# Kernel tuning notes

Measured on AMD Instinct MI355X. Metric: run time of the kernel, lower is better.

The kernel has to match this reference:

```python
import jax, jax.numpy as jnp
import numpy as np
from jax import lax

SEGMENTS = 64
KERNEL = 5


def setup_inputs() -> dict:
    key = jax.random.key(0)
    k1, k2, k3 = jax.random.split(key, 3)
    B, S, F = 4, 4096, 1024
    A6 = 512 * 6
    inp = jax.random.normal(k1, (B, S, F), dtype=jnp.float32)
    W = jax.random.normal(k2, (A6, F), dtype=jnp.float32) * (1.0 / np.sqrt(F))
    b = jax.random.normal(k3, (A6,), dtype=jnp.float32) * 0.01
    return {"inp": inp, "W": W, "b": b}


def reference(inp, W, b):
    # Fused projection: [B,S,F] @ [F,6A] -> [B,S,6A]
    x = jnp.einsum('bsf,af->bsa', inp, W) + b
    qry, key, val, seg, loc, out = jnp.split(x, 6, axis=2)  # each [B,S,A]
    B, S, A = out.shape

    # Global aggregated attention branch
    agg = qry.mean(axis=1)                              # [B,A]
    scores = jnp.einsum('ba,bsa->bs', agg, key)         # [B,S]
    w = jax.nn.softmax(scores, axis=1)                  # [B,S]
    ctx = jnp.einsum('bs,bsa->ba', w, val)              # [B,A]
    aggregated = ctx[:, None, :] * out                  # [B,S,A]

    # Segment max-pool branch
    nseg = S // SEGMENTS
    seg4 = seg.reshape(B, nseg, SEGMENTS, A)
    seg_max = seg4.max(axis=2, keepdims=True)           # [B,nseg,1,A]
    segment_max_pooled = (seg_max * out.reshape(B, nseg, SEGMENTS, A)).reshape(B, S, A)

    # Local sliding-window max-pool branch (stride 1, pad KERNEL//2, -inf padding)
    pad = KERNEL // 2
    local_max_pooled = lax.reduce_window(
        loc, -jnp.inf, lax.max,
        window_dimensions=(1, KERNEL, 1),
        window_strides=(1, 1, 1),
        padding=((0, 0), (pad, pad), (0, 0)))           # [B,S,A]

    return aggregated + segment_max_pooled + local_max_pooled
```

## Files before the change

### kernel.cpp

```cpp
#include <hip/hip_runtime.h>
#include <hip/hip_bf16.h>
#include <stdint.h>

#define B_    4
#define S_    4096
#define F_    1024
#define A_    512
#define N3_   1536
#define M_    16384

#define BM    256
#define BK    64
#define NT    (F_ / BK)
#define LDP   266

typedef __attribute__((ext_vector_type(8))) __bf16 bf16x8;
typedef __attribute__((ext_vector_type(4))) float  f32x4;

#define MFMA(a, b, c) __builtin_amdgcn_mfma_f32_16x16x32_bf16((a), (b), (c), 0, 0, 0)

__device__ __forceinline__ float bflo(unsigned int u) {
  union { unsigned int i; float f; } v; v.i = u << 16; return v.f;
}
__device__ __forceinline__ float bfhi(unsigned int u) {
  union { unsigned int i; float f; } v; v.i = u & 0xffff0000u; return v.f;
}
__device__ __forceinline__ float bf1(unsigned short u) {
  union { unsigned int i; float f; } v; v.i = ((unsigned int)u) << 16; return v.f;
}
__device__ __forceinline__ unsigned short bfc(float f) {
  return __builtin_bit_cast(unsigned short, __float2bfloat16(f));
}

__device__ __forceinline__ ushort4 cvt_bf4(float4 v) {
  ushort4 o;
  o.x = bfc(v.x); o.y = bfc(v.y); o.z = bfc(v.z); o.w = bfc(v.w);
  return o;
}

typedef __attribute__((address_space(3))) unsigned int lds_uint;
typedef const __attribute__((address_space(1))) unsigned int glob_uint;
__device__ __forceinline__ void lds_load16(const void* g, void* l) {
  __builtin_amdgcn_global_load_lds((glob_uint*)g, (lds_uint*)l, 16, 0, 0);
}

__global__ __launch_bounds__(256) void convert_mean_kernel(
    const float* __restrict__ inp, const float* __restrict__ W,
    unsigned short* __restrict__ inp_bf, unsigned short* __restrict__ w_bf,
    float* __restrict__ mu) {
  int blk = blockIdx.x;
  int t   = threadIdx.x;
  int r0  = blk * 32;
  int b   = r0 >> 12;
  float acc0 = 0.f, acc1 = 0.f, acc2 = 0.f, acc3 = 0.f;
  for (int r = 0; r < 32; r++) {
    size_t row = (size_t)(r0 + r);
    float4 v = ((const float4*)(inp + row * F_))[t];
    acc0 += v.x; acc1 += v.y; acc2 += v.z; acc3 += v.w;
    ((ushort4*)(inp_bf + row * F_))[t] = cvt_bf4(v);
  }
  atomicAdd(&mu[b * F_ + t * 4 + 0], acc0);
  atomicAdd(&mu[b * F_ + t * 4 + 1], acc1);
  atomicAdd(&mu[b * F_ + t * 4 + 2], acc2);
  atomicAdd(&mu[b * F_ + t * 4 + 3], acc3);

  const float* Wc = W + (size_t)N3_ * F_;
  const int n4 = (N3_ * F_) / 4;
  for (int i = blk * 256 + t; i < n4; i += 512 * 256) {
    ((ushort4*)w_bf)[i] = cvt_bf4(((const float4*)Wc)[i]);
  }
}

__global__ void agg_kernel(const float* __restrict__ mu, const float* __restrict__ W,
                           const float* __restrict__ bias, float* __restrict__ agg) {
  int gw = blockIdx.x * 4 + (threadIdx.x >> 6);
  int lane = threadIdx.x & 63;
  int b = gw >> 9, a = gw & 511;
  const float4* wr = (const float4*)(W + (size_t)a * F_);
  const float4* mr = (const float4*)(mu + b * F_);
  float s = 0.f;
#pragma unroll
  for (int k = 0; k < 4; k++) {
    float4 wv = wr[lane + 64 * k], mv = mr[lane + 64 * k];
    s += wv.x * mv.x + wv.y * mv.y + wv.z * mv.z + wv.w * mv.w;
  }
  for (int off = 32; off; off >>= 1) s += __shfl_down(s, off);
  if (lane == 0) agg[b * A_ + a] = s * (1.f / S_) + bias[a];
}

__global__ void v_kernel(const float* __restrict__ agg, const float* __restrict__ W,
                         const float* __restrict__ bias, float* __restrict__ v,
                         float* __restrict__ cvec) {
  int fc = blockIdx.x;
  int ac = blockIdx.y;
  int t = threadIdx.x;
  int f = fc * 256 + t;
  const float* Wk = W + (size_t)A_ * F_;
  float s0 = 0.f, s1 = 0.f, s2 = 0.f, s3 = 0.f;
  int a0 = ac * 64;
  for (int a = a0; a < a0 + 64; a++) {
    float wv = Wk[(size_t)a * F_ + f];
    s0 += agg[a] * wv;
    s1 += agg[A_ + a] * wv;
    s2 += agg[2 * A_ + a] * wv;
    s3 += agg[3 * A_ + a] * wv;
  }
  atomicAdd(&v[f], s0);
  atomicAdd(&v[F_ + f], s1);
  atomicAdd(&v[2 * F_ + f], s2);
  atomicAdd(&v[3 * F_ + f], s3);

  if (fc == 0 && ac == 0) {
    int bb = t >> 6, l = t & 63;
    float c = 0.f;
#pragma unroll
    for (int i = 0; i < 8; i++) c += agg[bb * A_ + l + 64 * i] * bias[A_ + l + 64 * i];
    for (int off = 32; off; off >>= 1) c += __shfl_down(c, off);
    if (l == 0) cvec[bb] = c;
  }
}

__global__ void scores_kernel(const unsigned short* __restrict__ inp_bf,
                              const float* __restrict__ v,
                              const float* __restrict__ cvec, float* __restrict__ scores) {
  int lane = threadIdx.x & 63;
  int row = blockIdx.x * 4 + (threadIdx.x >> 6);
  int b = row >> 12;
  const uint4* ip = (const uint4*)(inp_bf + (size_t)row * F_);
  const float4* vp = (const float4*)(v + b * F_);
  float s = 0.f;
#pragma unroll
  for (int k = 0; k < 2; k++) {
    uint4 x = ip[lane + 64 * k];
    float4 va = vp[(lane + 64 * k) * 2];
    float4 vb = vp[(lane + 64 * k) * 2 + 1];
    s += bflo(x.x) * va.x + bfhi(x.x) * va.y + bflo(x.y) * va.z + bfhi(x.y) * va.w +
         bflo(x.z) * vb.x + bfhi(x.z) * vb.y + bflo(x.w) * vb.z + bfhi(x.w) * vb.w;
  }
  for (int off = 32; off; off >>= 1) s += __shfl_down(s, off);
  if (lane == 0) scores[row] = s + cvec[b];
}

__global__ void softmax_kernel(float* __restrict__ sc) {
  __shared__ float red[256];
  int b = blockIdx.x, t = threadIdx.x;
  float* p = sc + b * S_;
  float vals[16];
  float m = -1e30f;
#pragma unroll
  for (int i = 0; i < 16; i++) { vals[i] = p[t + i * 256]; m = fmaxf(m, vals[i]); }
  red[t] = m; __syncthreads();
  for (int o = 128; o; o >>= 1) { if (t < o) red[t] = fmaxf(red[t], red[t + o]); __syncthreads(); }
  m = red[0]; __syncthreads();
  float sum = 0.f;
#pragma unroll
  for (int i = 0; i < 16; i++) { vals[i] = __expf(vals[i] - m); sum += vals[i]; }
  red[t] = sum; __syncthreads();
  for (int o = 128; o; o >>= 1) { if (t < o) red[t] += red[t + o]; __syncthreads(); }
  float inv = 1.f / red[0];
#pragma unroll
  for (int i = 0; i < 16; i++) p[t + i * 256] = vals[i] * inv;
}

__global__ void u_kernel(const unsigned short* __restrict__ inp_bf,
                         const float* __restrict__ w, float* __restrict__ u) {
  int b = blockIdx.z, fc = blockIdx.y, sc = blockIdx.x;
  int t = threadIdx.x;
  int f2 = fc * 512 + t * 2;
  int s0 = sc * 128;
  const float* wp = w + b * S_ + s0;
  const unsigned short* ip = inp_bf + ((size_t)(b * S_ + s0)) * F_ + f2;
  float a0 = 0.f, a1 = 0.f;
  for (int s = 0; s < 128; s++) {
    unsigned int xv = *(const unsigned int*)&ip[(size_t)s * F_];
    float ws = wp[s];
    a0 += ws * bflo(xv);
    a1 += ws * bfhi(xv);
  }
  atomicAdd(&u[b * F_ + f2], a0);
  atomicAdd(&u[b * F_ + f2 + 1], a1);
}

__global__ void ctx_kernel(const float* __restrict__ u, const float* __restrict__ W,
                           const float* __restrict__ bias, float* __restrict__ ctx) {
  int gw = blockIdx.x * 4 + (threadIdx.x >> 6);
  int lane = threadIdx.x & 63;
  int b = gw >> 9, a = gw & 511;
  const float4* wr = (const float4*)(W + (size_t)(2 * A_ + a) * F_);
  const float4* ur = (const float4*)(u + b * F_);
  float s = 0.f;
#pragma unroll
  for (int k = 0; k < 4; k++) {
    float4 wv = wr[lane + 64 * k], uv = ur[lane + 64 * k];
    s += wv.x * uv.x + wv.y * uv.y + wv.z * uv.z + wv.w * uv.w;
  }
  for (int off = 32; off; off >>= 1) s += __shfl_down(s, off);
  if (lane == 0) ctx[b * A_ + a] = s + bias[2 * A_ + a];
}

__global__ __launch_bounds__(512, 2) void gemm_fused(
    const __hip_bfloat16* __restrict__ Abf,
    const __hip_bfloat16* __restrict__ Wbf,
    const float* __restrict__ biasP,
    const float* __restrict__ ctx,
    float* __restrict__ out,
    unsigned short* __restrict__ sideLoc,
    float* __restrict__ sideGO) {
  extern __shared__ unsigned short smem[];
  unsigned short* ldsA = smem;
  unsigned short* ldsB = smem + 32768;
  unsigned short* Xt   = smem;
  float* segred = (float*)((char*)smem + 192 * LDP * 2);

  int bid = blockIdx.x;
  int swz = (bid & 7) * 64 + (bid >> 3);
  int mb = swz >> 3;
  int nb = swz & 7;

  int tid  = threadIdx.x;
  int lane = tid & 63;
  int wv   = tid >> 6;
  int wm   = wv >> 1;
  int wn   = wv & 1;
  int lo   = lane & 15, hi = lane >> 4, sw = lane & 7;

  int bir0 = (((hi * 16)      ^ (sw << 4)) >> 1);
  int bir1 = (((64 + hi * 16) ^ (sw << 4)) >> 1);

  const __hip_bfloat16* Ab = Abf + (size_t)mb * BM * F_;

  int srow = tid >> 3;
  int sel  = ((tid & 7) ^ (srow & 7)) * 8;
  int ldst = wv * 512;

  f32x4 acc[4][6];
#pragma unroll
  for (int i = 0; i < 4; i++)
#pragma unroll
    for (int j = 0; j < 6; j++) acc[i][j] = (f32x4){0.f, 0.f, 0.f, 0.f};

  int aBase = (wm * 64 + lo) * 64;
  int bBase = (wn * 96 + lo) * 64;

#define STG_A(kt_, buf_, r_)                                                              \
  lds_load16(Ab + (size_t)((r_) * 64 + srow) * F_ + (kt_) * BK + sel,                     \
             ldsA + (buf_) * 16384 + (r_) * 4096 + ldst)
#define STG_B(kt_, buf_, q_)                                                              \
  lds_load16(Wbf + (size_t)((q_) * 512 + nb * 64 + srow) * F_ + (kt_) * BK + sel,         \
             ldsB + (buf_) * 12288 + (q_) * 4096 + ldst)

  bf16x8 af[4][2], b01[2][2], b23[2][2], b45[2][2];

  STG_A(0, 0, 0); STG_A(0, 0, 1); STG_A(0, 0, 2); STG_A(0, 0, 3);
  STG_B(0, 0, 0); STG_B(0, 0, 1); STG_B(0, 0, 2);
  asm volatile("s_waitcnt vmcnt(0)" ::: "memory");
  __builtin_amdgcn_s_barrier();
#pragma unroll
  for (int i = 0; i < 4; i++) {
    af[i][0] = *(const bf16x8*)&ldsA[aBase + i * 1024 + bir0];
    af[i][1] = *(const bf16x8*)&ldsA[aBase + i * 1024 + bir1];
  }
#pragma unroll
  for (int j = 0; j < 2; j++) {
    b01[j][0] = *(const bf16x8*)&ldsB[bBase + j * 1024 + bir0];
    b01[j][1] = *(const bf16x8*)&ldsB[bBase + j * 1024 + bir1];
  }

  for (int kt = 0; kt < NT; ++kt) {
    int c = kt & 1, nx = c ^ 1;
    bool pf = (kt + 1 < NT);
    const unsigned short* lb  = ldsB + c * 12288;
    const unsigned short* lan = ldsA + nx * 16384;
    const unsigned short* lbn = ldsB + nx * 12288;

    if (pf) { STG_A(kt + 1, nx, 0); STG_A(kt + 1, nx, 1); STG_A(kt + 1, nx, 2); STG_A(kt + 1, nx, 3); }
    asm volatile("s_waitcnt lgkmcnt(0)" ::: "memory");
    __builtin_amdgcn_sched_barrier(0);
    __builtin_amdgcn_s_setprio(1);
#pragma unroll
    for (int i = 0; i < 4; i++)
#pragma unroll
      for (int j = 0; j < 2; j++) {
        acc[i][j] = MFMA(af[i][0], b01[j][0], acc[i][j]);
        acc[i][j] = MFMA(af[i][1], b01[j][1], acc[i][j]);
      }
    __builtin_amdgcn_s_setprio(0);
#pragma unroll
    for (int j = 0; j < 2; j++) {
      b23[j][0] = *(const bf16x8*)&lb[bBase + (2 + j) * 1024 + bir0];
      b23[j][1] = *(const bf16x8*)&lb[bBase + (2 + j) * 1024 + bir1];
    }
    __builtin_amdgcn_s_barrier();

    if (pf) { STG_B(kt + 1, nx, 0); STG_B(kt + 1, nx, 1); STG_B(kt + 1, nx, 2); }
    asm volatile("s_waitcnt lgkmcnt(0)" ::: "memory");
    __builtin_amdgcn_sched_barrier(0);
    __builtin_amdgcn_s_setprio(1);
#pragma unroll
    for (int i = 0; i < 4; i++)
#pragma unroll
      for (int j = 0; j < 2; j++) {
        acc[i][2 + j] = MFMA(af[i][0], b23[j][0], acc[i][2 + j]);
        acc[i][2 + j] = MFMA(af[i][1], b23[j][1], acc[i][2 + j]);
      }
    __builtin_amdgcn_s_setprio(0);
#pragma unroll
    for (int j = 0; j < 2; j++) {
      b45[j][0] = *(const bf16x8*)&lb[bBase + (4 + j) * 1024 + bir0];
      b45[j][1] = *(const bf16x8*)&lb[bBase + (4 + j) * 1024 + bir1];
    }
    __builtin_amdgcn_s_barrier();

    asm volatile("s_waitcnt lgkmcnt(0)" ::: "memory");
    __builtin_amdgcn_sched_barrier(0);
    __builtin_amdgcn_s_setprio(1);
#pragma unroll
    for (int i = 0; i < 4; i++)
#pragma unroll
      for (int j = 0; j < 2; j++) {
        acc[i][4 + j] = MFMA(af[i][0], b45[j][0], acc[i][4 + j]);
        acc[i][4 + j] = MFMA(af[i][1], b45[j][1], acc[i][4 + j]);
      }
    __builtin_amdgcn_s_setprio(0);
    if (pf) asm volatile("s_waitcnt vmcnt(0)" ::: "memory");
    __builtin_amdgcn_s_barrier();
    if (pf) {
#pragma unroll
      for (int i = 0; i < 4; i++) {
        af[i][0] = *(const bf16x8*)&lan[aBase + i * 1024 + bir0];
        af[i][1] = *(const bf16x8*)&lan[aBase + i * 1024 + bir1];
      }
#pragma unroll
      for (int j = 0; j < 2; j++) {
        b01[j][0] = *(const bf16x8*)&lbn[bBase + j * 1024 + bir0];
        b01[j][1] = *(const bf16x8*)&lbn[bBase + j * 1024 + bir1];
      }
    }
  }
#undef STG_A
#undef STG_B

  float bias_r[6];
#pragma unroll
  for (int fj = 0; fj < 6; fj++) {
    int cl = wn * 96 + fj * 16 + lo;
    bias_r[fj] = biasP[(cl >> 6) * 512 + nb * 64 + (cl & 63)];
  }
#pragma unroll
  for (int fi = 0; fi < 4; fi++) {
#pragma unroll
    for (int fj = 0; fj < 6; fj++) {
      int cl = wn * 96 + fj * 16 + lo;
      int r  = wm * 64 + fi * 16 + hi * 4;
      float v0 = acc[fi][fj][0] + bias_r[fj];
      float v1 = acc[fi][fj][1] + bias_r[fj];
      float v2 = acc[fi][fj][2] + bias_r[fj];
      float v3 = acc[fi][fj][3] + bias_r[fj];
      unsigned int u01 = (unsigned int)bfc(v0) | ((unsigned int)bfc(v1) << 16);
      unsigned int u23 = (unsigned int)bfc(v2) | ((unsigned int)bfc(v3) << 16);
      *(unsigned int*)&Xt[cl * LDP + r]     = u01;
      *(unsigned int*)&Xt[cl * LDP + r + 2] = u23;
    }
  }
  __syncthreads();

  if (tid < 256) {
    int seg = tid >> 6, c = tid & 63;
    int base = c * LDP + seg * 64;
    float m = -1e30f;
#pragma unroll
    for (int k = 0; k < 32; k++) {
      unsigned int u = *(const unsigned int*)&Xt[base + 2 * k];
      m = fmaxf(m, fmaxf(bflo(u), bfhi(u)));
    }
    segred[seg * 64 + c] = m;
  }
  __syncthreads();

  {
    int c  = lane;
    int r0 = wv * 32;
    int b  = mb >> 4;
    int gcol = nb * 64 + c;
    float g = ctx[b * 512 + gcol] + segred[(r0 >> 6) * 64 + c];
    int lbase = (64 + c) * LDP;
    int obase = (128 + c) * LDP;
    float lw0 = bf1(Xt[lbase + max(r0 - 2, 0)]);
    float lw1 = bf1(Xt[lbase + max(r0 - 1, 0)]);
    float lw2 = bf1(Xt[lbase + r0]);
    float lw3 = bf1(Xt[lbase + r0 + 1]);
    size_t obase_g = ((size_t)(mb * 256 + r0)) * 512 + gcol;
#pragma unroll
    for (int j = 0; j < 32; j++) {
      int rn = min(r0 + j + 2, 255);
      float lw4 = bf1(Xt[lbase + rn]);
      float lm = fmaxf(fmaxf(fmaxf(lw0, lw1), fmaxf(lw2, lw3)), lw4);
      float o = bf1(Xt[obase + r0 + j]);
      out[obase_g + (size_t)j * 512] = g * o + lm;
      lw0 = lw1; lw1 = lw2; lw2 = lw3; lw3 = lw4;
    }
  }

  if (tid < 256) {
    int rsel = tid >> 6, c = tid & 63;
    int r = (rsel < 2) ? rsel : (252 + rsel);
    int b = mb >> 4;
    float g = ctx[b * 512 + nb * 64 + c] + segred[(r >> 6) * 64 + c];
    float o = bf1(Xt[(128 + c) * LDP + r]);
    int gr = mb * 4 + rsel;
    sideLoc[gr * 512 + nb * 64 + c] = Xt[(64 + c) * LDP + r];
    sideGO[gr * 512 + nb * 64 + c]  = g * o;
  }
}

__global__ void fixup_kernel(const unsigned short* __restrict__ sideLoc,
                             const float* __restrict__ sideGO,
                             float* __restrict__ out) {
  int rb = blockIdx.x;
  int tb = rb & 15;
  int t = threadIdx.x;
  int rsel = t >> 6, cq = t & 63;
#pragma unroll
  for (int k = 0; k < 8; k++) {
    int c = cq * 8 + k;
    float miss;
    int rl;
    if (rsel == 0) {
      if (tb == 0) continue;
      miss = fmaxf(bf1(sideLoc[((rb - 1) * 4 + 2) * 512 + c]),
                   bf1(sideLoc[((rb - 1) * 4 + 3) * 512 + c]));
      rl = 0;
    } else if (rsel == 1) {
      if (tb == 0) continue;
      miss = bf1(sideLoc[((rb - 1) * 4 + 3) * 512 + c]);
      rl = 1;
    } else if (rsel == 2) {
      if (tb == 15) continue;
      miss = bf1(sideLoc[((rb + 1) * 4 + 0) * 512 + c]);
      rl = 254;
    } else {
      if (tb == 15) continue;
      miss = fmaxf(bf1(sideLoc[((rb + 1) * 4 + 0) * 512 + c]),
                   bf1(sideLoc[((rb + 1) * 4 + 1) * 512 + c]));
      rl = 255;
    }
    size_t oi = ((size_t)rb * 256 + rl) * 512 + c;
    float cand = sideGO[(rb * 4 + rsel) * 512 + c] + miss;
    out[oi] = fmaxf(out[oi], cand);
  }
}

extern "C" void kernel_launch(void* const* d_in, const int* in_sizes, int n_in,
                              void* d_out, int out_size, void* d_ws, size_t ws_size,
                              hipStream_t stream) {
  const float* inp  = (const float*)d_in[0];
  const float* W    = (const float*)d_in[1];
  const float* bias = (const float*)d_in[2];
  float* out = (float*)d_out;
  char* ws = (char*)d_ws;

  const size_t INP_OFF  = 0;
  const size_t W_OFF    = 33554432;
  const size_t MU_OFF   = 36700160;
  const size_t U_OFF    = MU_OFF + 16384;
  const size_t V_OFF    = U_OFF + 16384;
  const size_t CV_OFF   = V_OFF + 16384;
  const size_t AGG_OFF  = CV_OFF + 256;
  const size_t CTX_OFF  = AGG_OFF + 8192;
  const size_t SC_OFF   = CTX_OFF + 8192;
  const size_t SL_OFF   = SC_OFF + 65536;
  const size_t SG_OFF   = SL_OFF + 262144;

  unsigned short* inp_bf = (unsigned short*)(ws + INP_OFF);
  unsigned short* w_bf   = (unsigned short*)(ws + W_OFF);
  float* mu     = (float*)(ws + MU_OFF);
  float* u      = (float*)(ws + U_OFF);
  float* v      = (float*)(ws + V_OFF);
  float* cvec   = (float*)(ws + CV_OFF);
  float* agg    = (float*)(ws + AGG_OFF);
  float* ctx    = (float*)(ws + CTX_OFF);
  float* scores = (float*)(ws + SC_OFF);
  unsigned short* sideLoc = (unsigned short*)(ws + SL_OFF);
  float* sideGO = (float*)(ws + SG_OFF);

  hipFuncSetAttribute(reinterpret_cast<const void*>(gemm_fused),
                      hipFuncAttributeMaxDynamicSharedMemorySize, 114688);

  hipMemsetAsync(ws + MU_OFF, 0, 3 * 16384 + 256, stream);
  convert_mean_kernel<<<512, 256, 0, stream>>>(inp, W, inp_bf, w_bf, mu);
  agg_kernel<<<512, 256, 0, stream>>>(mu, W, bias, agg);
  v_kernel<<<dim3(4, 8), 256, 0, stream>>>(agg, W, bias, v, cvec);
  scores_kernel<<<4096, 256, 0, stream>>>(inp_bf, v, cvec, scores);
  softmax_kernel<<<4, 256, 0, stream>>>(scores);
  u_kernel<<<dim3(32, 2, 4), 256, 0, stream>>>(inp_bf, scores, u);
  ctx_kernel<<<512, 256, 0, stream>>>(u, W, bias, ctx);
  gemm_fused<<<512, 512, 114688, stream>>>((const __hip_bfloat16*)inp_bf,
                                           (const __hip_bfloat16*)w_bf,
                                           bias + 3 * A_, ctx, out, sideLoc, sideGO);
  fixup_kernel<<<64, 256, 0, stream>>>(sideLoc, sideGO, out);
}
```

Baseline: 126.8 us.

## Fuse scores, softmax and weighted sum into chunked online-softmax kernels

Replaces the separate scores, softmax and u kernels with a per-chunk kernel that computes scores, a local max/exp and a partial weighted sum. A small combine kernel then rescales the partials with a global max and normaliser. The per-batch bias constant is dropped because softmax ignores a constant shift. This removes one full pass over the bf16 input, the 4-block serial softmax and the atomics. The cost is an extra partial buffer and a combine step.

```diff
diff --git a/kernel.cpp b/kernel.cpp
--- a/kernel.cpp
+++ b/kernel.cpp
@@ -15,9 +15,9 @@
 #define LDP   266
 
 typedef __attribute__((ext_vector_type(8))) __bf16 bf16x8;
-typedef __attribute__((ext_vector_type(4))) float  f32x4;
 
 #define MFMA(a, b, c) __builtin_amdgcn_mfma_f32_16x16x32_bf16((a), (b), (c), 0, 0, 0)
+typedef __attribute__((ext_vector_type(4))) float f32x4;
 
 __device__ __forceinline__ float bflo(unsigned int u) {
   union { unsigned int i; float f; } v; v.i = u << 16; return v.f;
@@ -31,7 +31,6 @@
 __device__ __forceinline__ unsigned short bfc(float f) {
   return __builtin_bit_cast(unsigned short, __float2bfloat16(f));
 }
-
 __device__ __forceinline__ ushort4 cvt_bf4(float4 v) {
   ushort4 o;
   o.x = bfc(v.x); o.y = bfc(v.y); o.z = bfc(v.z); o.w = bfc(v.w);
@@ -89,8 +88,7 @@
 }
 
 __global__ void v_kernel(const float* __restrict__ agg, const float* __restrict__ W,
-                         const float* __restrict__ bias, float* __restrict__ v,
-                         float* __restrict__ cvec) {
+                         float* __restrict__ v) {
   int fc = blockIdx.x;
   int ac = blockIdx.y;
   int t = threadIdx.x;
@@ -109,76 +107,77 @@
   atomicAdd(&v[F_ + f], s1);
   atomicAdd(&v[2 * F_ + f], s2);
   atomicAdd(&v[3 * F_ + f], s3);
-
-  if (fc == 0 && ac == 0) {
-    int bb = t >> 6, l = t & 63;
-    float c = 0.f;
-#pragma unroll
-    for (int i = 0; i < 8; i++) c += agg[bb * A_ + l + 64 * i] * bias[A_ + l + 64 * i];
-    for (int off = 32; off; off >>= 1) c += __shfl_down(c, off);
-    if (l == 0) cvec[bb] = c;
-  }
-}
-
-__global__ void scores_kernel(const unsigned short* __restrict__ inp_bf,
-                              const float* __restrict__ v,
-                              const float* __restrict__ cvec, float* __restrict__ scores) {
-  int lane = threadIdx.x & 63;
-  int row = blockIdx.x * 4 + (threadIdx.x >> 6);
-  int b = row >> 12;
-  const uint4* ip = (const uint4*)(inp_bf + (size_t)row * F_);
+}
+
+__global__ __launch_bounds__(256) void scores_u_kernel(
+    const unsigned short* __restrict__ inp_bf, const float* __restrict__ v,
+    float* __restrict__ uP, float* __restrict__ mlzl) {
+  int blk = blockIdx.x;
+  int b = blk >> 6, ch = blk & 63;
+  int s0 = ch * 64;
+  int t = threadIdx.x, lane = t & 63, wv = t >> 6;
+  __shared__ float sc[64];
+  __shared__ float wsl[64];
+
   const float4* vp = (const float4*)(v + b * F_);
-  float s = 0.f;
-#pragma unroll
-  for (int k = 0; k < 2; k++) {
-    uint4 x = ip[lane + 64 * k];
-    float4 va = vp[(lane + 64 * k) * 2];
-    float4 vb = vp[(lane + 64 * k) * 2 + 1];
-    s += bflo(x.x) * va.x + bfhi(x.x) * va.y + bflo(x.y) * va.z + bfhi(x.y) * va.w +
-         bflo(x.z) * vb.x + bfhi(x.z) * vb.y + bflo(x.w) * vb.z + bfhi(x.w) * vb.w;
-  }
-  for (int off = 32; off; off >>= 1) s += __shfl_down(s, off);
-  if (lane == 0) scores[row] = s + cvec[b];
-}
-
-__global__ void softmax_kernel(float* __restrict__ sc) {
-  __shared__ float red[256];
-  int b = blockIdx.x, t = threadIdx.x;
-  float* p = sc + b * S_;
-  float vals[16];
+  float4 va0 = vp[lane * 2], va1 = vp[lane * 2 + 1];
+  float4 vb0 = vp[(lane + 64) * 2], vb1 = vp[(lane + 64) * 2 + 1];
+#pragma unroll
+  for (int i = 0; i < 16; i++) {
+    int r = wv * 16 + i;
+    const uint4* ip = (const uint4*)(inp_bf + ((size_t)(b * S_ + s0 + r)) * F_);
+    uint4 x0 = ip[lane], x1 = ip[lane + 64];
+    float s = bflo(x0.x) * va0.x + bfhi(x0.x) * va0.y + bflo(x0.y) * va0.z + bfhi(x0.y) * va0.w +
+              bflo(x0.z) * va1.x + bfhi(x0.z) * va1.y + bflo(x0.w) * va1.z + bfhi(x0.w) * va1.w +
+              bflo(x1.x) * vb0.x + bfhi(x1.x) * vb0.y + bflo(x1.y) * vb0.z + bfhi(x1.y) * vb0.w +
+              bflo(x1.z) * vb1.x + bfhi(x1.z) * vb1.y + bflo(x1.w) * vb1.z + bfhi(x1.w) * vb1.w;
+    for (int off = 32; off; off >>= 1) s += __shfl_down(s, off);
+    if (lane == 0) sc[r] = s;
+  }
+  __syncthreads();
+
   float m = -1e30f;
 #pragma unroll
-  for (int i = 0; i < 16; i++) { vals[i] = p[t + i * 256]; m = fmaxf(m, vals[i]); }
-  red[t] = m; __syncthreads();
-  for (int o = 128; o; o >>= 1) { if (t < o) red[t] = fmaxf(red[t], red[t + o]); __syncthreads(); }
-  m = red[0]; __syncthreads();
-  float sum = 0.f;
-#pragma unroll
-  for (int i = 0; i < 16; i++) { vals[i] = __expf(vals[i] - m); sum += vals[i]; }
-  red[t] = sum; __syncthreads();
-  for (int o = 128; o; o >>= 1) { if (t < o) red[t] += red[t + o]; __syncthreads(); }
-  float inv = 1.f / red[0];
-#pragma unroll
-  for (int i = 0; i < 16; i++) p[t + i * 256] = vals[i] * inv;
-}
-
-__global__ void u_kernel(const unsigned short* __restrict__ inp_bf,
-                         const float* __restrict__ w, float* __restrict__ u) {
-  int b = blockIdx.z, fc = blockIdx.y, sc = blockIdx.x;
-  int t = threadIdx.x;
-  int f2 = fc * 512 + t * 2;
-  int s0 = sc * 128;
-  const float* wp = w + b * S_ + s0;
-  const unsigned short* ip = inp_bf + ((size_t)(b * S_ + s0)) * F_ + f2;
-  float a0 = 0.f, a1 = 0.f;
-  for (int s = 0; s < 128; s++) {
-    unsigned int xv = *(const unsigned int*)&ip[(size_t)s * F_];
-    float ws = wp[s];
-    a0 += ws * bflo(xv);
-    a1 += ws * bfhi(xv);
-  }
-  atomicAdd(&u[b * F_ + f2], a0);
-  atomicAdd(&u[b * F_ + f2 + 1], a1);
+  for (int i = 0; i < 64; i++) m = fmaxf(m, sc[i]);
+  if (t < 64) wsl[t] = __expf(sc[t] - m);
+  __syncthreads();
+
+  {
+    const unsigned short* xp = inp_bf + ((size_t)(b * S_ + s0)) * F_ + t * 4;
+    float a0 = 0.f, a1 = 0.f, a2 = 0.f, a3 = 0.f;
+    for (int s = 0; s < 64; s++) {
+      uint2 xv = *(const uint2*)&xp[(size_t)s * F_];
+      float w = wsl[s];
+      a0 += w * bflo(xv.x); a1 += w * bfhi(xv.x);
+      a2 += w * bflo(xv.y); a3 += w * bfhi(xv.y);
+    }
+    float4 o; o.x = a0; o.y = a1; o.z = a2; o.w = a3;
+    *(float4*)&uP[(size_t)blk * 1024 + t * 4] = o;
+  }
+  if (t == 0) {
+    float Z = 0.f;
+#pragma unroll
+    for (int i = 0; i < 64; i++) Z += wsl[i];
+    mlzl[blk * 2] = m; mlzl[blk * 2 + 1] = Z;
+  }
+}
+
+__global__ void ufin_kernel(const float* __restrict__ uP, const float* __restrict__ mlzl,
+                            float* __restrict__ u) {
+  int b = blockIdx.x >> 2, fs = blockIdx.x & 3;
+  int f = fs * 256 + threadIdx.x;
+  float M = -1e30f;
+#pragma unroll
+  for (int i = 0; i < 64; i++) M = fmaxf(M, mlzl[(b * 64 + i) * 2]);
+  float Z = 0.f;
+#pragma unroll
+  for (int i = 0; i < 64; i++) Z += __expf(mlzl[(b * 64 + i) * 2] - M) * mlzl[(b * 64 + i) * 2 + 1];
+  float acc = 0.f;
+  for (int ch = 0; ch < 64; ch++) {
+    float sc = __expf(mlzl[(b * 64 + ch) * 2] - M);
+    acc += sc * uP[(size_t)(b * 64 + ch) * 1024 + f];
+  }
+  u[b * F_ + f] = acc / Z;
 }
 
 __global__ void ctx_kernel(const float* __restrict__ u, const float* __restrict__ W,
@@ -370,8 +369,8 @@
     float m = -1e30f;
 #pragma unroll
     for (int k = 0; k < 32; k++) {
-      unsigned int u = *(const unsigned int*)&Xt[base + 2 * k];
-      m = fmaxf(m, fmaxf(bflo(u), bfhi(u)));
+      unsigned int uu = *(const unsigned int*)&Xt[base + 2 * k];
+      m = fmaxf(m, fmaxf(bflo(uu), bfhi(uu)));
     }
     segred[seg * 64 + c] = m;
   }
@@ -464,35 +463,34 @@
   const size_t MU_OFF   = 36700160;
   const size_t U_OFF    = MU_OFF + 16384;
   const size_t V_OFF    = U_OFF + 16384;
-  const size_t CV_OFF   = V_OFF + 16384;
-  const size_t AGG_OFF  = CV_OFF + 256;
+  const size_t AGG_OFF  = V_OFF + 16384;
   const size_t CTX_OFF  = AGG_OFF + 8192;
-  const size_t SC_OFF   = CTX_OFF + 8192;
-  const size_t SL_OFF   = SC_OFF + 65536;
+  const size_t SL_OFF   = CTX_OFF + 8192;
   const size_t SG_OFF   = SL_OFF + 262144;
+  const size_t UP_OFF   = SG_OFF + 524288;
+  const size_t ML_OFF   = UP_OFF + 1048576;
 
   unsigned short* inp_bf = (unsigned short*)(ws + INP_OFF);
   unsigned short* w_bf   = (unsigned short*)(ws + W_OFF);
   float* mu     = (float*)(ws + MU_OFF);
   float* u      = (float*)(ws + U_OFF);
   float* v      = (float*)(ws + V_OFF);
-  float* cvec   = (float*)(ws + CV_OFF);
   float* agg    = (float*)(ws + AGG_OFF);
   float* ctx    = (float*)(ws + CTX_OFF);
-  float* scores = (float*)(ws + SC_OFF);
   unsigned short* sideLoc = (unsigned short*)(ws + SL_OFF);
   float* sideGO = (float*)(ws + SG_OFF);
+  float* uP     = (float*)(ws + UP_OFF);
+  float* mlzl   = (float*)(ws + ML_OFF);
 
   hipFuncSetAttribute(reinterpret_cast<const void*>(gemm_fused),
                       hipFuncAttributeMaxDynamicSharedMemorySize, 114688);
 
-  hipMemsetAsync(ws + MU_OFF, 0, 3 * 16384 + 256, stream);
+  hipMemsetAsync(ws + MU_OFF, 0, 3 * 16384, stream);
   convert_mean_kernel<<<512, 256, 0, stream>>>(inp, W, inp_bf, w_bf, mu);
   agg_kernel<<<512, 256, 0, stream>>>(mu, W, bias, agg);
-  v_kernel<<<dim3(4, 8), 256, 0, stream>>>(agg, W, bias, v, cvec);
-  scores_kernel<<<4096, 256, 0, stream>>>(inp_bf, v, cvec, scores);
-  softmax_kernel<<<4, 256, 0, stream>>>(scores);
-  u_kernel<<<dim3(32, 2, 4), 256, 0, stream>>>(inp_bf, scores, u);
+  v_kernel<<<dim3(4, 8), 256, 0, stream>>>(agg, W, v);
+  scores_u_kernel<<<256, 256, 0, stream>>>(inp_bf, v, uP, mlzl);
+  ufin_kernel<<<16, 256, 0, stream>>>(uP, mlzl, u);
   ctx_kernel<<<512, 256, 0, stream>>>(u, W, bias, ctx);
   gemm_fused<<<512, 512, 114688, stream>>>((const __hip_bfloat16*)inp_bf,
                                            (const __hip_bfloat16*)w_bf,
```

Measured after the change: 128.2 us. No clear change (+1.1%).
